# Optimization experiments

Measured on AMD Instinct MI355X. Metric: run time of the kernel, lower is better.

## Reference

```python
import jax, jax.numpy as jnp
import numpy as np

N_QUBITS = 12
N_LAYERS = 8
BATCH = 1024
DIM = 2 ** N_QUBITS


def _apply_rx(state, theta, wire):
    # state: (B, 2**n) complex64; theta: scalar or (B,)
    B = state.shape[0]
    A, C = 2 ** wire, 2 ** (N_QUBITS - wire - 1)
    s = state.reshape(B, A, 2, C)
    half = theta * 0.5
    c = jnp.reshape(jnp.cos(half), (-1, 1, 1))
    sn = jnp.reshape(jnp.sin(half), (-1, 1, 1))
    s0, s1 = s[:, :, 0], s[:, :, 1]
    out = jnp.stack([c * s0 - 1j * sn * s1, c * s1 - 1j * sn * s0], axis=2)
    return out.reshape(B, DIM)


def _apply_rz(state, theta, wire):
    B = state.shape[0]
    A, C = 2 ** wire, 2 ** (N_QUBITS - wire - 1)
    s = state.reshape(B, A, 2, C)
    half = theta * 0.5
    ph0 = jnp.reshape(jnp.cos(half) - 1j * jnp.sin(half), (-1, 1, 1))  # e^{-i t/2}
    out = jnp.stack([ph0 * s[:, :, 0], jnp.conj(ph0) * s[:, :, 1]], axis=2)
    return out.reshape(B, DIM)


def _apply_cnot(state, control):
    # CNOT on wires (control, control+1)
    B = state.shape[0]
    A, C = 2 ** control, 2 ** (N_QUBITS - control - 2)
    s = state.reshape(B, A, 2, 2, C)
    s1 = s[:, :, 1][:, :, ::-1]  # control=1 -> flip target bit
    out = jnp.stack([s[:, :, 0], s1], axis=2)
    return out.reshape(B, DIM)


def _layer(state, p):
    # one variational layer: CNOT ladder then RX/RZ per qubit; p: (2*n,)
    for i in range(N_QUBITS - 1):
        state = _apply_cnot(state, i)
    for i in range(N_QUBITS):
        state = _apply_rx(state, p[2 * i], i)
        state = _apply_rz(state, p[2 * i + 1], i)
    return state


def _pauliz_expvals(state):
    B = state.shape[0]
    probs = state.real ** 2 + state.imag ** 2  # (B, 2**n)
    zs = []
    for w in range(N_QUBITS):
        A, C = 2 ** w, 2 ** (N_QUBITS - w - 1)
        p = probs.reshape(B, A, 2, C)
        zs.append((p[:, :, 0] - p[:, :, 1]).sum(axis=(1, 2)))
    return jnp.stack(zs, axis=1)  # (B, n_qubits)


def setup_inputs() -> dict:
    key = jax.random.key(0)
    k1, k2, k3 = jax.random.split(key, 3)
    x = jax.random.uniform(k1, (BATCH, N_QUBITS), dtype=jnp.float32)
    qnn_params = jax.random.normal(k2, (N_LAYERS, 2 * N_QUBITS), dtype=jnp.float32)
    linear_weights = jax.random.normal(k3, (N_QUBITS, N_QUBITS), dtype=jnp.float32)
    return {"x": x, "qnn_params": qnn_params, "linear_weights": linear_weights}


def reference(x, qnn_params, linear_weights):
    B = x.shape[0]
    # |0...0> initial state, batched
    state = jnp.zeros((B, DIM), dtype=jnp.complex64).at[:, 0].set(1.0)
    # data encoding: RX(pi * x_i) per wire (batched angles)
    for i in range(N_QUBITS):
        state = _apply_rx(state, x[:, i] * jnp.pi, i)
    # variational layers
    state, _ = jax.lax.scan(lambda s, p: (_layer(s, p), None), state, qnn_params)
    z = _pauliz_expvals(state)  # (B, n_qubits)
    y = jax.nn.relu(z @ linear_weights)
    return jnp.sum(y, axis=-1)  # (B,)
```

## Files before the change

kernel.cpp:

```cpp
#include <hip/hip_runtime.h>

#define NQ 12
#define NLAYERS 8
#define BATCH 1024

typedef float v2f __attribute__((ext_vector_type(2)));


constexpr int hbit(int m){ int h=0; while(m>>(h+1)) ++h; return 1<<h; }

__device__ __forceinline__ v2f vsplat(float s){ v2f v; v.x=s; v.y=s; return v; }
__device__ __forceinline__ v2f vswap(v2f v){ return __builtin_shufflevector(v, v, 1, 0); }
template<int S> __device__ __forceinline__ v2f msw(v2f v){ if constexpr (S) return vswap(v); else return v; }
__device__ __forceinline__ v2f vfma(v2f a, v2f b, v2f c){ return __builtin_elementwise_fma(a,b,c); }

template<int S>
__device__ __forceinline__ void rx_upd(v2f& ro, v2f& io, v2f r, v2f i, v2f pr, v2f pi,
                                       v2f hc2, v2f hs2, v2f ns2){
    ro = vfma(hc2, r, hs2*msw<S>(pi));
    io = vfma(hc2, i, ns2*msw<S>(pr));
}

__device__ __forceinline__ v2f bperm2(int addr, v2f v){
    v2f r;
    r.x = __int_as_float(__builtin_amdgcn_ds_bpermute(addr, __float_as_int(v.x)));
    r.y = __int_as_float(__builtin_amdgcn_ds_bpermute(addr, __float_as_int(v.y)));
    return r;
}

template<int CTRL>
__device__ __forceinline__ float dpp1(float v){
    int i = __float_as_int(v);
    return __int_as_float(__builtin_amdgcn_update_dpp(i, i, CTRL, 0xF, 0xF, true));
}
template<int LM>
__device__ __forceinline__ float dppx(float v){
    static_assert(LM >= 1 && LM <= 15, "dpp xor range");
    constexpr int h = (LM >> 2) & 3;
    float r = v;
    if constexpr (h == 1 || h == 2) r = dpp1<0x141>(r);
    if constexpr (h == 3 || h == 2) r = dpp1<0x140>(r);
    constexpr int st = (h==1)?7 : (h==2)?8 : (h==3)?15 : 0;
    constexpr int q = (LM ^ st) & 3;
    if constexpr (q == 1) r = dpp1<0xB1>(r);
    if constexpr (q == 2) r = dpp1<0x4E>(r);
    if constexpr (q == 3) r = dpp1<0x1B>(r);
    return r;
}

template<int JM>
__device__ __forceinline__ void rx_local(v2f (&re2)[16], v2f (&im2)[16], v2f hc2, v2f hs2, v2f ns2){
    if constexpr (JM == 1){
        #pragma unroll
        for (int t=0;t<16;++t){
            v2f r=re2[t], i=im2[t];
            rx_upd<1>(re2[t], im2[t], r, i, r, i, hc2, hs2, ns2);
        }
    } else {
        constexpr int m = JM>>1, HB = hbit(m), S = JM&1;
        #pragma unroll
        for (int t=0;t<16;++t){
            if (t & HB) continue;
            const int t2 = t ^ m;
            v2f ru=re2[t], iu=im2[t], rv=re2[t2], iv=im2[t2];
            rx_upd<S>(re2[t],  im2[t],  ru, iu, rv, iv, hc2, hs2, ns2);
            rx_upd<S>(re2[t2], im2[t2], rv, iv, ru, iu, hc2, hs2, ns2);
        }
    }
}

template<int W>
__device__ __forceinline__ void rx_canon(v2f (&re2)[16], v2f (&im2)[16], float hc, float hs, int lane){
    const v2f hc2 = vsplat(hc), hs2 = vsplat(hs), ns2 = vsplat(-hs);
    if constexpr (W >= 1 && W <= 2){
        const int addr = ((lane ^ (1<<(6-W))) & 63) << 2;
        #pragma unroll
        for (int t=0;t<16;++t){
            v2f r=re2[t], i=im2[t];
            v2f pi = bperm2(addr, i);
            v2f pr = bperm2(addr, r);
            rx_upd<0>(re2[t], im2[t], r, i, pr, pi, hc2, hs2, ns2);
        }
    } else if constexpr (W >= 3 && W <= 6){
        constexpr int LM = 1<<(6-W);
        #pragma unroll
        for (int t=0;t<16;++t){
            v2f r=re2[t], i=im2[t];
            v2f pr, pi;
            float a0=dppx<LM>(r.x), a1=dppx<LM>(r.y);
            float b0=dppx<LM>(i.x), b1=dppx<LM>(i.y);
            pr.x=a0; pr.y=a1; pi.x=b0; pi.y=b1;
            rx_upd<0>(re2[t], im2[t], r, i, pr, pi, hc2, hs2, ns2);
        }
    } else {
        rx_local<(1<<(11-W))>(re2, im2, hc2, hs2, ns2);
    }
}

template<int W>
__device__ __forceinline__ void rz_gate(v2f (&re2)[16], v2f (&im2)[16], float hc, float hs,
                                        int lane, int wv){
    float hp;
    if constexpr (W == 0)      hp = wv ? -hs : hs;
    else if constexpr (W <= 6) hp = ((lane >> (6-W)) & 1) ? -hs : hs;
    else                       hp = hs;
    v2f A;
    if constexpr (W == 11){ A.x = hp; A.y = -hp; } else { A = vsplat(hp); }
    const v2f nA = -A;
    const v2f hc2 = vsplat(hc);
    #pragma unroll
    for (int t=0;t<16;++t){
        bool odd = false;
        if constexpr (W >= 7 && W <= 10) odd = (t >> (10-W)) & 1;
        const v2f SV = odd ? nA : A;
        const v2f SN = odd ? A : nA;
        v2f r = re2[t], i = im2[t];
        re2[t] = vfma(hc2, r, SV*i);
        im2[t] = vfma(hc2, i, SN*r);
    }
}

__device__ __forceinline__ void exch_write(const v2f (&re2)[16], const v2f (&im2)[16],
                                           int lane, int wv, float4* lds4){
    float4* wr = lds4 + (wv*16)*64 + lane;
    #pragma unroll
    for (int u=0;u<8;++u){
        float4 fr; fr.x=re2[2*u].x; fr.y=re2[2*u].y; fr.z=re2[2*u+1].x; fr.w=re2[2*u+1].y;
        float4 fi; fi.x=im2[2*u].x; fi.y=im2[2*u].y; fi.z=im2[2*u+1].x; fi.w=im2[2*u+1].y;
        wr[u*64]     = fr;
        wr[(8+u)*64] = fi;
    }
}

__device__ __forceinline__ void perm_rx0(v2f (&re2)[16], v2f (&im2)[16],
                                         float hc, float hs, int lane, int wv,
                                         const float4* lds4){
    const v2f hc2 = vsplat(hc), hs2 = vsplat(hs), ns2 = vsplat(-hs);
    const int sl = ((lane ^ (lane>>1)) & 63) ^ (wv<<5);
    const int rb = (lane & 1) << 2;
    const float4* rdS = lds4 + (wv*16)*64 + sl;
    const float4* rdP = lds4 + ((wv^1)*16)*64 + (sl^32);
    #pragma unroll
    for (int u=0;u<8;++u){
        const int row = (u ^ (u>>1)) ^ rb;
        float4 Fr = rdS[row*64], Fi = rdS[(row+8)*64];
        float4 Gr = rdP[row*64], Gi = rdP[(row+8)*64];
        v2f ar,ai,br,bi, pr,pi,qr,qi;
        if ((u & 1) == 0){
            ar.x=Fr.x; ar.y=Fr.y;  br.x=Fr.w; br.y=Fr.z;
            ai.x=Fi.x; ai.y=Fi.y;  bi.x=Fi.w; bi.y=Fi.z;
            pr.x=Gr.x; pr.y=Gr.y;  qr.x=Gr.w; qr.y=Gr.z;
            pi.x=Gi.x; pi.y=Gi.y;  qi.x=Gi.w; qi.y=Gi.z;
        } else {
            ar.x=Fr.z; ar.y=Fr.w;  br.x=Fr.y; br.y=Fr.x;
            ai.x=Fi.z; ai.y=Fi.w;  bi.x=Fi.y; bi.y=Fi.x;
            pr.x=Gr.z; pr.y=Gr.w;  qr.x=Gr.y; qr.y=Gr.x;
            pi.x=Gi.z; pi.y=Gi.w;  qi.x=Gi.y; qi.y=Gi.x;
        }
        rx_upd<0>(re2[2*u],   im2[2*u],   ar, ai, pr, pi, hc2, hs2, ns2);
        rx_upd<0>(re2[2*u+1], im2[2*u+1], br, bi, qr, qi, hc2, hs2, ns2);
    }
}

__device__ __forceinline__ void init_rx0(v2f (&re2)[16], v2f (&im2)[16],
                                         float hc, float hs, int lane, int wv, float4* lds4){
    const v2f hc2 = vsplat(hc), hs2 = vsplat(hs), ns2 = vsplat(-hs);
    exch_write(re2, im2, lane, wv, lds4);
    __syncthreads();
    const float4* rd = lds4 + ((wv^1)*16)*64 + lane;
    #pragma unroll
    for (int u=0;u<8;++u){
        float4 Fr = rd[u*64], Fi = rd[(u+8)*64];
        v2f prl,pil,prh,pih;
        prl.x=Fr.x; prl.y=Fr.y; prh.x=Fr.z; prh.y=Fr.w;
        pil.x=Fi.x; pil.y=Fi.y; pih.x=Fi.z; pih.y=Fi.w;
        rx_upd<0>(re2[2*u],   im2[2*u],   re2[2*u],   im2[2*u],   prl, pil, hc2, hs2, ns2);
        rx_upd<0>(re2[2*u+1], im2[2*u+1], re2[2*u+1], im2[2*u+1], prh, pih, hc2, hs2, ns2);
    }
    __syncthreads();
}

template<int W>
__device__ __forceinline__ void gates_w(v2f (&re2)[16], v2f (&im2)[16],
                                        const float4* __restrict__ tb, int lane, int wv){
    const float4 t = tb[W];
    rx_canon<W>(re2, im2, t.x, t.y, lane);
    rz_gate<W>(re2, im2, t.z, t.w, lane, wv);
    if constexpr (W+1 < NQ) gates_w<W+1>(re2, im2, tb, lane, wv);
}

template<int W>
__device__ __forceinline__ void init_w(v2f (&re2)[16], v2f (&im2)[16],
                                       const float* __restrict__ xb, int lane){
    float hs, hc;
    __sincosf(xb[W]*1.5707963267948966f, &hs, &hc);
    rx_canon<W>(re2, im2, hc, hs, lane);
    if constexpr (W+1 < NQ) init_w<W+1>(re2, im2, xb, lane);
}

__global__ void prep_kernel(const float* __restrict__ P, float4* __restrict__ tbl){
    const int i = threadIdx.x;
    if (i < NLAYERS*NQ){
        float4 v;
        __sincosf(P[2*i]   * 0.5f, &v.y, &v.x);
        __sincosf(P[2*i+1] * 0.5f, &v.w, &v.z);
        tbl[i] = v;
    }
}

__global__ __launch_bounds__(128, 2) void qnn_kernel(const float* __restrict__ x,
                                                     const float4* __restrict__ tbl,
                                                     const float* __restrict__ Wm,
                                                     float* __restrict__ out)
{
    __shared__ float4 lds4[2*16*64];
    const int lane = threadIdx.x & 63;
    const int wv   = threadIdx.x >> 6;
    const int b    = blockIdx.x;

    v2f re2[16], im2[16];
    #pragma unroll
    for (int t=0;t<16;++t){ re2[t] = vsplat(0.f); im2[t] = vsplat(0.f); }
    if (threadIdx.x == 0) re2[0].x = 1.0f;

    const float* xb = x + b*NQ;
    init_w<1>(re2, im2, xb, lane);
    {
        float hs0, hc0;
        __sincosf(xb[0]*1.5707963267948966f, &hs0, &hc0);
        init_rx0(re2, im2, hc0, hs0, lane, wv, lds4);
    }

    #pragma unroll 1
    for (int l = 0; l < NLAYERS; ++l){
        const float4* tb = tbl + l*NQ;
        const float4 t0 = tb[0];
        exch_write(re2, im2, lane, wv, lds4);
        __syncthreads();
        perm_rx0(re2, im2, t0.x, t0.y, lane, wv, lds4);
        rz_gate<0>(re2, im2, t0.z, t0.w, lane, wv);
        gates_w<1>(re2, im2, tb, lane, wv);
        __syncthreads();
    }

    v2f S = vsplat(0.f), S7 = vsplat(0.f), S8 = vsplat(0.f), S9 = vsplat(0.f), S10 = vsplat(0.f);
    #pragma unroll
    for (int t=0;t<16;++t){
        v2f p2 = __builtin_elementwise_fma(re2[t], re2[t], im2[t]*im2[t]);
        S += p2;
        S7  += (t&8)? -p2 : p2;
        S8  += (t&4)? -p2 : p2;
        S9  += (t&2)? -p2 : p2;
        S10 += (t&1)? -p2 : p2;
    }
    const float s0 = S.x + S.y;

    float z[12];
    z[0] = wv ? -s0 : s0;
    #pragma unroll
    for (int w=1; w<=6; ++w) z[w] = ((lane >> (6-w)) & 1) ? -s0 : s0;
    z[7]  = S7.x + S7.y;
    z[8]  = S8.x + S8.y;
    z[9]  = S9.x + S9.y;
    z[10] = S10.x + S10.y;
    z[11] = S.x - S.y;

    #pragma unroll
    for (int m=1; m<64; m<<=1){
        #pragma unroll
        for (int w=0; w<12; ++w) z[w] += __shfl_xor(z[w], m, 64);
    }

    float* sh = (float*)lds4;
    if (lane == 0){
        #pragma unroll
        for (int w=0; w<12; ++w) sh[wv*12 + w] = z[w];
    }
    __syncthreads();
    if (wv == 0){
        float t = 0.f;
        if (lane < 12){
            #pragma unroll
            for (int w=0; w<12; ++w){
                float zz = sh[w] + sh[12+w];
                t = fmaf(zz, Wm[w*12 + lane], t);
            }
            t = fmaxf(t, 0.f);
        }
        #pragma unroll
        for (int m=1; m<16; m<<=1) t += __shfl_xor(t, m, 64);
        if (lane == 0) out[b] = t;
    }
}

extern "C" void kernel_launch(void* const* d_in, const int* in_sizes, int n_in,
                              void* d_out, int out_size, void* d_ws, size_t ws_size,
                              hipStream_t stream) {
    const float* x  = (const float*)d_in[0];
    const float* P  = (const float*)d_in[1];
    const float* Wm = (const float*)d_in[2];
    float* out = (float*)d_out;
    float4* tbl = (float4*)d_ws;
    prep_kernel<<<1, 128, 0, stream>>>(P, tbl);
    qnn_kernel<<<BATCH, 128, 0, stream>>>(x, tbl, Wm, out);
}
```

Measured before the change: 88.60 us.

## Fold all per-layer RZ gates into one combined diagonal phase multiply

Each layer's twelve RZ gates commute with the RX gates on other wires, so they are moved to the end of the layer and merged into one diagonal phase per amplitude. The phase is split into a lane/wave part (alpha, one sincos per thread) and a per-register part taken from a table that the prep kernel fills with the cos/sin of summed angles for wires 7–11. This replaces twelve full passes over the 32 register vectors with a single complex multiply per element. In exchange it adds table loads, a per-thread sincos, and a slightly different floating-point rounding order.

```diff
diff --git a/kernel.cpp b/kernel.cpp
--- a/kernel.cpp
+++ b/kernel.cpp
@@ -94,29 +94,6 @@
         }
     } else {
         rx_local<(1<<(11-W))>(re2, im2, hc2, hs2, ns2);
-    }
-}
-
-template<int W>
-__device__ __forceinline__ void rz_gate(v2f (&re2)[16], v2f (&im2)[16], float hc, float hs,
-                                        int lane, int wv){
-    float hp;
-    if constexpr (W == 0)      hp = wv ? -hs : hs;
-    else if constexpr (W <= 6) hp = ((lane >> (6-W)) & 1) ? -hs : hs;
-    else                       hp = hs;
-    v2f A;
-    if constexpr (W == 11){ A.x = hp; A.y = -hp; } else { A = vsplat(hp); }
-    const v2f nA = -A;
-    const v2f hc2 = vsplat(hc);
-    #pragma unroll
-    for (int t=0;t<16;++t){
-        bool odd = false;
-        if constexpr (W >= 7 && W <= 10) odd = (t >> (10-W)) & 1;
-        const v2f SV = odd ? nA : A;
-        const v2f SN = odd ? A : nA;
-        v2f r = re2[t], i = im2[t];
-        re2[t] = vfma(hc2, r, SV*i);
-        im2[t] = vfma(hc2, i, SN*r);
     }
 }
 
@@ -182,11 +159,10 @@
 
 template<int W>
 __device__ __forceinline__ void gates_w(v2f (&re2)[16], v2f (&im2)[16],
-                                        const float4* __restrict__ tb, int lane, int wv){
-    const float4 t = tb[W];
+                                        const float2* __restrict__ tb, int lane){
+    const float2 t = tb[W];
     rx_canon<W>(re2, im2, t.x, t.y, lane);
-    rz_gate<W>(re2, im2, t.z, t.w, lane, wv);
-    if constexpr (W+1 < NQ) gates_w<W+1>(re2, im2, tb, lane, wv);
+    if constexpr (W+1 < NQ) gates_w<W+1>(re2, im2, tb, lane);
 }
 
 template<int W>
@@ -198,18 +174,41 @@
     if constexpr (W+1 < NQ) init_w<W+1>(re2, im2, xb, lane);
 }
 
-__global__ void prep_kernel(const float* __restrict__ P, float4* __restrict__ tbl){
+__global__ void prep_kernel(const float* __restrict__ P, float* __restrict__ ws){
     const int i = threadIdx.x;
-    if (i < NLAYERS*NQ){
-        float4 v;
-        __sincosf(P[2*i]   * 0.5f, &v.y, &v.x);
-        __sincosf(P[2*i+1] * 0.5f, &v.w, &v.z);
-        tbl[i] = v;
+    float2* tRX = (float2*)ws;
+    float*  tTH = ws + 192;
+    float4* tJ  = (float4*)(ws + 256);
+    if (i < 96){
+        const int l = i/12, w = i%12;
+        float2 v; __sincosf(P[l*24 + 2*w]*0.5f, &v.y, &v.x);
+        tRX[i] = v;
+    }
+    if (i < 64){
+        const int l = i>>3, w = i&7;
+        tTH[i] = (w < 7) ? P[l*24 + 2*w + 1]*0.5f : 0.f;
+    }
+    {
+        const int l = i>>4, t = i&15;
+        float br[2], bi[2];
+        #pragma unroll
+        for (int k=0;k<2;++k){
+            const int j = 2*t + k;
+            float beta = 0.f;
+            #pragma unroll
+            for (int w=7; w<12; ++w){
+                const float th = P[l*24 + 2*w + 1]*0.5f;
+                beta += ((j >> (11-w)) & 1) ? th : -th;
+            }
+            __sincosf(beta, &bi[k], &br[k]);
+        }
+        float4 v; v.x=br[0]; v.y=br[1]; v.z=bi[0]; v.w=bi[1];
+        tJ[i] = v;
     }
 }
 
 __global__ __launch_bounds__(128, 2) void qnn_kernel(const float* __restrict__ x,
-                                                     const float4* __restrict__ tbl,
+                                                     const float* __restrict__ ws,
                                                      const float* __restrict__ Wm,
                                                      float* __restrict__ out)
 {
@@ -218,6 +217,10 @@
     const int wv   = threadIdx.x >> 6;
     const int b    = blockIdx.x;
 
+    const float2* tRX = (const float2*)ws;
+    const float*  tTH = ws + 192;
+    const float4* tJ  = (const float4*)(ws + 256);
+
     v2f re2[16], im2[16];
     #pragma unroll
     for (int t=0;t<16;++t){ re2[t] = vsplat(0.f); im2[t] = vsplat(0.f); }
@@ -233,13 +236,34 @@
 
     #pragma unroll 1
     for (int l = 0; l < NLAYERS; ++l){
-        const float4* tb = tbl + l*NQ;
-        const float4 t0 = tb[0];
+        const float2* tb = tRX + l*12;
+        const float2 t0 = tb[0];
         exch_write(re2, im2, lane, wv, lds4);
         __syncthreads();
         perm_rx0(re2, im2, t0.x, t0.y, lane, wv, lds4);
-        rz_gate<0>(re2, im2, t0.z, t0.w, lane, wv);
-        gates_w<1>(re2, im2, tb, lane, wv);
+        gates_w<1>(re2, im2, tb, lane);
+
+        const float* th = tTH + l*8;
+        float alpha = wv ? th[0] : -th[0];
+        #pragma unroll
+        for (int w=1; w<=6; ++w)
+            alpha += ((lane >> (6-w)) & 1) ? th[w] : -th[w];
+        float sa, ca;
+        __sincosf(alpha, &sa, &ca);
+        const v2f vca = vsplat(ca), vsa = vsplat(sa), vna = vsplat(-sa);
+        const float4* tj = tJ + l*16;
+        #pragma unroll
+        for (int t=0;t<16;++t){
+            const float4 J = tj[t];
+            v2f jr; jr.x=J.x; jr.y=J.y;
+            v2f ji; ji.x=J.z; ji.y=J.w;
+            const v2f cr = vfma(vca, jr, vna*ji);
+            const v2f ci = vfma(vca, ji, vsa*jr);
+            const v2f nci = -ci;
+            const v2f r = re2[t], m = im2[t];
+            re2[t] = vfma(r, cr, m*nci);
+            im2[t] = vfma(m, cr, r*ci);
+        }
         __syncthreads();
     }
 
@@ -300,7 +324,7 @@
     const float* P  = (const float*)d_in[1];
     const float* Wm = (const float*)d_in[2];
     float* out = (float*)d_out;
-    float4* tbl = (float4*)d_ws;
-    prep_kernel<<<1, 128, 0, stream>>>(P, tbl);
-    qnn_kernel<<<BATCH, 128, 0, stream>>>(x, tbl, Wm, out);
-}
+    float* ws  = (float*)d_ws;
+    prep_kernel<<<1, 128, 0, stream>>>(P, ws);
+    qnn_kernel<<<BATCH, 128, 0, stream>>>(x, ws, Wm, out);
+}
```

Result: faster. 71.97 us (-18.8%).
